# Kernel optimization log

Measured on AMD Instinct MI355X. Metric: run time of the kernel, lower is better.

## Reference

```python
import jax, jax.numpy as jnp
import numpy as np

B, L = 1, 384
D_EDGE, D_BIAS, N_HEAD, D_HEAD = 128, 64, 4, 48
INF = 1000000.0
SCALE = 1.0 / np.sqrt(D_HEAD)
EPS = 1e-5


def _layernorm(x, g, b):
    mu = jnp.mean(x, axis=-1, keepdims=True)
    var = jnp.mean(jnp.square(x - mu), axis=-1, keepdims=True)
    return (x - mu) * jax.lax.rsqrt(var + EPS) * g + b


def _rope(x, pos):
    # x: [B, n, L, h, d], pos: [B, L] integer positions along the attended (i/j) axis
    half = x.shape[-1] // 2
    inv_freq = 1.0 / (10000.0 ** (jnp.arange(half, dtype=jnp.float32) / half))
    ang = pos.astype(jnp.float32)[..., None] * inv_freq          # [B, L, half]
    cos = jnp.cos(ang)[:, None, :, None, :]                       # [B,1,L,1,half]
    sin = jnp.sin(ang)[:, None, :, None, :]
    x1, x2 = jnp.split(x, 2, axis=-1)
    return jnp.concatenate([x1 * cos - x2 * sin, x1 * sin + x2 * cos], axis=-1)


def setup_inputs() -> dict:
    key = jax.random.key(0)
    ks = jax.random.split(key, 10)
    s = 0.02
    return {
        "edge": jax.random.normal(ks[0], (B, L, L, D_EDGE), jnp.float32),
        "bias": jax.random.normal(ks[1], (B, L, L, D_BIAS), jnp.float32),
        "edge_pos": jnp.arange(B * L, dtype=jnp.int32).reshape(B, L),
        "edge_mask": jnp.ones((B, L, L), jnp.float32),
        "ln_e_g": jnp.ones((D_EDGE,), jnp.float32),
        "ln_e_b": jnp.zeros((D_EDGE,), jnp.float32),
        "ln_b_g": jnp.ones((D_BIAS,), jnp.float32),
        "ln_b_b": jnp.zeros((D_BIAS,), jnp.float32),
        "Wq": jax.random.normal(ks[2], (D_EDGE, N_HEAD * D_HEAD), jnp.float32) * s,
        "Wk": jax.random.normal(ks[3], (D_EDGE, N_HEAD * D_HEAD), jnp.float32) * s,
        "Wv": jax.random.normal(ks[4], (D_EDGE, N_HEAD * D_HEAD), jnp.float32) * s,
        "Wb": jax.random.normal(ks[5], (D_BIAS, N_HEAD), jnp.float32) * s,
        "Wg": jax.random.normal(ks[6], (D_EDGE, N_HEAD * D_HEAD), jnp.float32) * s,
        "bg": jnp.zeros((N_HEAD * D_HEAD,), jnp.float32),
        "Wo": jax.random.normal(ks[7], (N_HEAD * D_HEAD, D_EDGE), jnp.float32) * s,
    }


def reference(edge, bias, edge_pos, edge_mask, ln_e_g, ln_e_b, ln_b_g, ln_b_b,
              Wq, Wk, Wv, Wb, Wg, bg, Wo):
    # is_row=True: swap the two residue axes of the pair representation
    e = jnp.transpose(edge, (0, 2, 1, 3))
    bi = jnp.transpose(bias, (0, 2, 1, 3))
    e = _layernorm(e, ln_e_g, ln_e_b)
    bi = _layernorm(bi, ln_b_g, ln_b_b)

    def proj(x, W):
        return (x @ W).reshape(B, L, L, N_HEAD, D_HEAD)

    q = proj(e, Wq)                      # [B, n, i, h, d]
    k = proj(e, Wk)
    v = proj(e, Wv)
    q = _rope(q, edge_pos)
    k = _rope(k, edge_pos)
    b_h = bi @ Wb                        # [B, i, j, h]
    gate = jax.nn.sigmoid(proj(e, Wg) + bg.reshape(1, 1, 1, N_HEAD, D_HEAD))

    q = q * SCALE
    k = k / L
    attn = jnp.einsum('bnihk,bnjhk->bijh', q, k) + b_h
    attn = jax.nn.softmax(attn, axis=-2)                 # softmax over j (dim -2)
    attn = attn + (INF * (edge_mask - 1.0))[..., None]    # post-softmax additive mask

    out = jnp.einsum('bijh,bnjhd->bnihd', attn, v)        # [B, n, i, h, d]
    out = gate * out
    out = out.reshape(B, L, L, N_HEAD * D_HEAD) @ Wo      # [B, n, i, d_edge]
    return jnp.transpose(out, (0, 2, 1, 3))               # undo row permute
```

## Files before the change

### kernel.cpp

```cpp
#include <hip/hip_runtime.h>
#include <hip/hip_bf16.h>


#define LQ 384
#define DE 128
#define DBI 64
#define NH 4
#define DH 48
#define NPOS (LQ*LQ)
#define KQK (LQ*DH)
#define LDSS 72

typedef __attribute__((ext_vector_type(8))) short short8;
typedef __attribute__((ext_vector_type(4))) float f32x4;
typedef unsigned short u16;
typedef unsigned int u32;

__device__ __forceinline__ float b2f(u16 u) {
  union { u32 i; float f; } v; v.i = ((u32)u) << 16; return v.f;
}
__device__ __forceinline__ u16 f2b(float f) {
  __hip_bfloat16 h = __float2bfloat16(f);
  return __builtin_bit_cast(unsigned short, h);
}
__device__ __forceinline__ float wred_sum(float v) {
  #pragma unroll
  for (int o = 32; o; o >>= 1) v += __shfl_down(v, o);
  return __shfl(v, 0);
}

template<int NF>
__device__ __forceinline__ void gemm_loop(
    const u16* __restrict__ Ag, long lda,
    const u16* __restrict__ Bg, long ldb,
    int kTiles, u16* sA, u16* sB, f32x4 (&acc)[2][NF])
{
  const int t = threadIdx.x;
  const int w = t >> 6, lane = t & 63, quad = lane >> 4, l16 = lane & 15;
  for (int kt = 0; kt < kTiles; ++kt) {
    const u16* As = Ag + (long)kt * 64;
    #pragma unroll
    for (int r = 0; r < 4; ++r) {
      int id = t + r * 256;
      int row = id >> 3, c8 = (id & 7) * 8;
      *(uint4*)(sA + row * LDSS + c8) = *(const uint4*)(As + (long)row * lda + c8);
    }
    const u16* Bs = Bg + (long)kt * 64;
    #pragma unroll
    for (int r = 0; r < (NF * 128 + 255) / 256; ++r) {
      int id = t + r * 256;
      if (id < NF * 128) {
        int row = id >> 3, c8 = (id & 7) * 8;
        *(uint4*)(sB + row * LDSS + c8) = *(const uint4*)(Bs + (long)row * ldb + c8);
      }
    }
    __syncthreads();
    #pragma unroll
    for (int kk = 0; kk < 64; kk += 32) {
      short8 a0 = *(const short8*)(sA + (w * 32 + l16) * LDSS + kk + quad * 8);
      short8 a1 = *(const short8*)(sA + (w * 32 + 16 + l16) * LDSS + kk + quad * 8);
      #pragma unroll
      for (int f = 0; f < NF; ++f) {
        short8 bf = *(const short8*)(sB + (f * 16 + l16) * LDSS + kk + quad * 8);
        acc[0][f] = __builtin_amdgcn_mfma_f32_16x16x32_bf16(a0, bf, acc[0][f], 0, 0, 0);
        acc[1][f] = __builtin_amdgcn_mfma_f32_16x16x32_bf16(a1, bf, acc[1][f], 0, 0, 0);
      }
    }
    __syncthreads();
  }
}

__device__ __forceinline__ void gemm_loop_mul(
    const u16* __restrict__ A1, const u16* __restrict__ A2, long lda,
    const u16* __restrict__ Bg, long ldb,
    int kTiles, u16* sA, u16* sB, f32x4 (&acc)[2][4])
{
  const int t = threadIdx.x;
  const int w = t >> 6, lane = t & 63, quad = lane >> 4, l16 = lane & 15;
  for (int kt = 0; kt < kTiles; ++kt) {
    #pragma unroll
    for (int r = 0; r < 4; ++r) {
      int id = t + r * 256;
      int row = id >> 3, c8 = (id & 7) * 8;
      long off = (long)row * lda + kt * 64 + c8;
      union { u16 s[8]; uint4 v; } ua, ub, ur;
      ua.v = *(const uint4*)(A1 + off);
      ub.v = *(const uint4*)(A2 + off);
      #pragma unroll
      for (int q2 = 0; q2 < 8; ++q2) ur.s[q2] = f2b(b2f(ua.s[q2]) * b2f(ub.s[q2]));
      *(uint4*)(sA + row * LDSS + c8) = ur.v;
    }
    #pragma unroll
    for (int r = 0; r < 2; ++r) {
      int id = t + r * 256;
      int row = id >> 3, c8 = (id & 7) * 8;
      *(uint4*)(sB + row * LDSS + c8) = *(const uint4*)(Bg + (long)row * ldb + kt * 64 + c8);
    }
    __syncthreads();
    #pragma unroll
    for (int kk = 0; kk < 64; kk += 32) {
      short8 a0 = *(const short8*)(sA + (w * 32 + l16) * LDSS + kk + quad * 8);
      short8 a1 = *(const short8*)(sA + (w * 32 + 16 + l16) * LDSS + kk + quad * 8);
      #pragma unroll
      for (int f = 0; f < 4; ++f) {
        short8 bf = *(const short8*)(sB + (f * 16 + l16) * LDSS + kk + quad * 8);
        acc[0][f] = __builtin_amdgcn_mfma_f32_16x16x32_bf16(a0, bf, acc[0][f], 0, 0, 0);
        acc[1][f] = __builtin_amdgcn_mfma_f32_16x16x32_bf16(a1, bf, acc[1][f], 0, 0, 0);
      }
    }
    __syncthreads();
  }
}

__global__ __launch_bounds__(256) void k_prep_w(
    const float* __restrict__ Wq, const float* __restrict__ Wk,
    const float* __restrict__ Wv, const float* __restrict__ Wg,
    const float* __restrict__ Wo, u16* __restrict__ WT, u16* __restrict__ WoT)
{
  int idx = blockIdx.x * 256 + threadIdx.x;
  if (idx < 768 * 128) {
    int col = idx >> 7, c = idx & 127;
    int which = col / 192, wi = col % 192;
    const float* W = (which == 0) ? Wq : (which == 1) ? Wk : (which == 2) ? Wv : Wg;
    WT[(long)col * 128 + c] = f2b(W[(long)c * 192 + wi]);
  }
  if (idx < 128 * 192) {
    int c = idx / 192, col = idx % 192;
    WoT[(long)c * 192 + col] = f2b(Wo[(long)col * 128 + c]);
  }
}

__global__ __launch_bounds__(256) void k_ln_e(
    const float* __restrict__ edge, const float* __restrict__ g,
    const float* __restrict__ b, u16* __restrict__ e_ln)
{
  int w = threadIdx.x >> 6, lane = threadIdx.x & 63;
  long p = (long)blockIdx.x * 4 + w;
  int n = (int)(p / LQ), i2 = (int)(p % LQ);
  const float* src = edge + ((long)i2 * LQ + n) * DE;
  float2 x = *(const float2*)(src + lane * 2);
  float mu = wred_sum(x.x + x.y) * (1.f / 128.f);
  float ms = wred_sum(x.x * x.x + x.y * x.y) * (1.f / 128.f);
  float r = rsqrtf(ms - mu * mu + 1e-5f);
  int c = lane * 2;
  u16 y0 = f2b((x.x - mu) * r * g[c] + b[c]);
  u16 y1 = f2b((x.y - mu) * r * g[c + 1] + b[c + 1]);
  *(u32*)(e_ln + p * DE + c) = (u32)y0 | ((u32)y1 << 16);
}

__global__ __launch_bounds__(256) void k_bias(
    const float* __restrict__ bias, const float* __restrict__ g,
    const float* __restrict__ b, const float* __restrict__ Wb,
    float* __restrict__ logits)
{
  int w = threadIdx.x >> 6, lane = threadIdx.x & 63;
  long q = (long)blockIdx.x * 4 + w;
  int i = (int)(q / LQ), j = (int)(q % LQ);
  float x = bias[((long)j * LQ + i) * DBI + lane];
  float mu = wred_sum(x) * (1.f / 64.f);
  float ms = wred_sum(x * x) * (1.f / 64.f);
  float r = rsqrtf(ms - mu * mu + 1e-5f);
  float y = (x - mu) * r * g[lane] + b[lane];
  #pragma unroll
  for (int h = 0; h < 4; ++h) {
    float v = y * Wb[lane * 4 + h];
    #pragma unroll
    for (int o = 32; o; o >>= 1) v += __shfl_down(v, o);
    if (lane == 0) logits[((long)h * LQ + i) * LQ + j] = v;
  }
}

__global__ __launch_bounds__(256) void k_proj(
    const u16* __restrict__ e_ln, const u16* __restrict__ WT,
    const int* __restrict__ edge_pos, const float* __restrict__ bg,
    u16* __restrict__ q_buf, u16* __restrict__ k_buf,
    u16* __restrict__ vT, u16* __restrict__ gate)
{
  __shared__ u16 sA[128 * LDSS];
  __shared__ u16 sB[48 * LDSS];
  __shared__ float sC[128 * 49];
  int nt = blockIdx.x;
  long mt = blockIdx.y;
  int which = nt >> 2, h = nt & 3;
  f32x4 acc[2][3] = {};
  gemm_loop<3>(e_ln + mt * 128 * DE, DE, WT + (long)nt * 48 * DE, DE, 2, sA, sB, acc);
  const int t = threadIdx.x;
  const int w = t >> 6, lane = t & 63, quad = lane >> 4, l16 = lane & 15;
  #pragma unroll
  for (int rf = 0; rf < 2; ++rf)
    #pragma unroll
    for (int f = 0; f < 3; ++f)
      #pragma unroll
      for (int r = 0; r < 4; ++r)
        sC[(w * 32 + rf * 16 + quad * 4 + r) * 49 + f * 16 + l16] = acc[rf][f][r];
  __syncthreads();
  long pbase = mt * 128;
  int n = (int)(pbase / LQ);
  int i2base = (int)(pbase % LQ);
  if (which < 2) {
    float scl = (which == 0) ? 0.14433756729740643f : (1.0f / 384.0f);
    u16* dst = (which == 0) ? q_buf : k_buf;
    int row = t >> 1, half = t & 1;
    int i2 = i2base + row;
    float posf = (float)edge_pos[i2];
    long base = ((long)(h * LQ + i2) * LQ + n) * DH;
    #pragma unroll
    for (int kd = 0; kd < 24; kd += 2) {
      u16 y2[2];
      #pragma unroll
      for (int u = 0; u < 2; ++u) {
        int d = half * 24 + kd + u;
        int dd = (d < 24) ? d : d - 24;
        float ang = posf * exp2f((float)dd * (-13.287712379549449f / 24.f));
        float sn = sinf(ang), cs = cosf(ang);
        float x1 = sC[row * 49 + dd], x2 = sC[row * 49 + dd + 24];
        float y = (d < 24) ? (x1 * cs - x2 * sn) : (x1 * sn + x2 * cs);
        y2[u] = f2b(y * scl);
      }
      *(u32*)(dst + base + half * 24 + kd) = (u32)y2[0] | ((u32)y2[1] << 16);
    }
  } else if (which == 2) {
    for (int e = t; e < 6144; e += 256) {
      int d = e >> 7, row = e & 127;
      vT[((long)h * KQK + n * DH + d) * LQ + (i2base + row)] = f2b(sC[row * 49 + d]);
    }
  } else {
    for (int e = t; e < 6144; e += 256) {
      int row = e / 48, d = e - row * 48;
      float xx = sC[row * 49 + d] + bg[h * DH + d];
      gate[(pbase + row) * 192 + h * DH + d] = f2b(1.f / (1.f + expf(-xx)));
    }
  }
}

__global__ __launch_bounds__(256) void k_qk(
    const u16* __restrict__ q_buf, const u16* __restrict__ k_buf,
    float* __restrict__ logits)
{
  __shared__ u16 sA[128 * LDSS];
  __shared__ u16 sB[48 * LDSS];
  int nt = blockIdx.x & 7, s = blockIdx.x >> 3;
  int mt = blockIdx.y, h = blockIdx.z;
  f32x4 acc[2][3] = {};
  gemm_loop<3>(q_buf + ((long)h * LQ + mt * 128) * KQK + s * 2304, KQK,
               k_buf + ((long)h * LQ + nt * 48) * KQK + s * 2304, KQK,
               36, sA, sB, acc);
  const int t = threadIdx.x;
  const int w = t >> 6, lane = t & 63, quad = lane >> 4, l16 = lane & 15;
  #pragma unroll
  for (int rf = 0; rf < 2; ++rf)
    #pragma unroll
    for (int f = 0; f < 3; ++f)
      #pragma unroll
      for (int r = 0; r < 4; ++r) {
        int row = mt * 128 + w * 32 + rf * 16 + quad * 4 + r;
        int col = nt * 48 + f * 16 + l16;
        atomicAdd(logits + ((long)h * LQ + row) * LQ + col, acc[rf][f][r]);
      }
}

__global__ __launch_bounds__(256) void k_softmax(
    const float* __restrict__ logits, const float* __restrict__ mask,
    u16* __restrict__ attn)
{
  int w = threadIdx.x >> 6, lane = threadIdx.x & 63;
  long row = (long)blockIdx.x * 4 + w;
  int i = (int)(row % LQ);
  const float* src = logits + row * LQ;
  float v[6];
  float mx = -1e30f;
  #pragma unroll
  for (int j0 = 0; j0 < 6; ++j0) { v[j0] = src[lane + j0 * 64]; mx = fmaxf(mx, v[j0]); }
  #pragma unroll
  for (int o = 32; o; o >>= 1) mx = fmaxf(mx, __shfl_down(mx, o));
  mx = __shfl(mx, 0);
  float s = 0.f;
  #pragma unroll
  for (int j0 = 0; j0 < 6; ++j0) { v[j0] = expf(v[j0] - mx); s += v[j0]; }
  s = wred_sum(s);
  float inv = 1.f / s;
  #pragma unroll
  for (int j0 = 0; j0 < 6; ++j0) {
    int j = lane + j0 * 64;
    float p = v[j0] * inv + 1.0e6f * (mask[(long)i * LQ + j] - 1.f);
    attn[row * LQ + j] = f2b(p);
  }
}

__global__ __launch_bounds__(256) void k_av(
    const u16* __restrict__ attn, const u16* __restrict__ vT,
    u16* __restrict__ out_buf)
{
  __shared__ u16 sA[128 * LDSS];
  __shared__ u16 sB[48 * LDSS];
  int nt = blockIdx.x, mt = blockIdx.y, h = blockIdx.z;
  f32x4 acc[2][3] = {};
  gemm_loop<3>(attn + ((long)h * LQ + mt * 128) * LQ, LQ,
               vT + ((long)h * KQK + nt * DH) * LQ, LQ,
               6, sA, sB, acc);
  const int t = threadIdx.x;
  const int w = t >> 6, lane = t & 63, quad = lane >> 4, l16 = lane & 15;
  #pragma unroll
  for (int rf = 0; rf < 2; ++rf)
    #pragma unroll
    for (int f = 0; f < 3; ++f)
      #pragma unroll
      for (int r = 0; r < 4; ++r) {
        int i = mt * 128 + w * 32 + rf * 16 + quad * 4 + r;
        int d = f * 16 + l16;
        out_buf[((long)nt * LQ + i) * 192 + h * DH + d] = f2b(acc[rf][f][r]);
      }
}

__global__ __launch_bounds__(256) void k_out(
    const u16* __restrict__ out_buf, const u16* __restrict__ gate,
    const u16* __restrict__ WoT, float* __restrict__ outp)
{
  __shared__ u16 sA[128 * LDSS];
  __shared__ u16 sB[64 * LDSS];
  int nt = blockIdx.x;
  long mt = blockIdx.y;
  f32x4 acc[2][4] = {};
  gemm_loop_mul(out_buf + mt * 128 * 192, gate + mt * 128 * 192, 192,
                WoT + (long)nt * 64 * 192, 192, 3, sA, sB, acc);
  const int t = threadIdx.x;
  const int w = t >> 6, lane = t & 63, quad = lane >> 4, l16 = lane & 15;
  long pbase = mt * 128;
  int n = (int)(pbase / LQ), ibase = (int)(pbase % LQ);
  #pragma unroll
  for (int rf = 0; rf < 2; ++rf)
    #pragma unroll
    for (int f = 0; f < 4; ++f)
      #pragma unroll
      for (int r = 0; r < 4; ++r) {
        int row = w * 32 + rf * 16 + quad * 4 + r;
        int c = nt * 64 + f * 16 + l16;
        outp[((long)(ibase + row) * LQ + n) * DE + c] = acc[rf][f][r];
      }
}

extern "C" void kernel_launch(void* const* d_in, const int* in_sizes, int n_in,
                              void* d_out, int out_size, void* d_ws, size_t ws_size,
                              hipStream_t stream)
{
  const float* edge   = (const float*)d_in[0];
  const float* bias   = (const float*)d_in[1];
  const int*   epos   = (const int*)d_in[2];
  const float* mask   = (const float*)d_in[3];
  const float* ln_e_g = (const float*)d_in[4];
  const float* ln_e_b = (const float*)d_in[5];
  const float* ln_b_g = (const float*)d_in[6];
  const float* ln_b_b = (const float*)d_in[7];
  const float* Wq = (const float*)d_in[8];
  const float* Wk = (const float*)d_in[9];
  const float* Wv = (const float*)d_in[10];
  const float* Wb = (const float*)d_in[11];
  const float* Wg = (const float*)d_in[12];
  const float* bg = (const float*)d_in[13];
  const float* Wo = (const float*)d_in[14];
  float* outp = (float*)d_out;

  char* ws = (char*)d_ws;
  const size_t SZ = (size_t)NPOS * 192 * 2;
  u16* e_ln    = (u16*)ws;
  u16* out_buf = (u16*)ws;
  u16* q_buf   = (u16*)(ws + SZ);
  u16* k_buf   = (u16*)(ws + 2 * SZ);
  u16* vTb     = (u16*)(ws + 3 * SZ);
  u16* gateb   = (u16*)(ws + 4 * SZ);
  float* logits= (float*)(ws + 5 * SZ);
  u16* attn    = (u16*)(ws + 5 * SZ + 2359296);
  u16* WT      = (u16*)(ws + 5 * SZ + 2359296 + 1179648);
  u16* WoT     = (u16*)(ws + 5 * SZ + 2359296 + 1179648 + 196608);

  k_prep_w<<<dim3(384), dim3(256), 0, stream>>>(Wq, Wk, Wv, Wg, Wo, WT, WoT);
  k_ln_e<<<dim3(36864), dim3(256), 0, stream>>>(edge, ln_e_g, ln_e_b, e_ln);
  k_bias<<<dim3(36864), dim3(256), 0, stream>>>(bias, ln_b_g, ln_b_b, Wb, logits);
  k_proj<<<dim3(16, 1152), dim3(256), 0, stream>>>(e_ln, WT, epos, bg, q_buf, k_buf, vTb, gateb);
  k_qk<<<dim3(64, 3, 4), dim3(256), 0, stream>>>(q_buf, k_buf, logits);
  k_softmax<<<dim3(384), dim3(256), 0, stream>>>(logits, mask, attn);
  k_av<<<dim3(384, 3, 4), dim3(256), 0, stream>>>(attn, vTb, out_buf);
  k_out<<<dim3(2, 1152), dim3(256), 0, stream>>>(out_buf, gateb, WoT, outp);
}
```

Measured before the change: 684.8 us.

## Enlarge GEMM tiles, reuse A tile across projections, precompute RoPE tables

```diff
diff --git a/kernel.cpp b/kernel.cpp
--- a/kernel.cpp
+++ b/kernel.cpp
@@ -5,11 +5,9 @@
 #define LQ 384
 #define DE 128
 #define DBI 64
-#define NH 4
 #define DH 48
 #define NPOS (LQ*LQ)
 #define KQK (LQ*DH)
-#define LDSS 72
 
 typedef __attribute__((ext_vector_type(8))) short short8;
 typedef __attribute__((ext_vector_type(4))) float f32x4;
@@ -29,84 +27,39 @@
   return __shfl(v, 0);
 }
 
-template<int NF>
-__device__ __forceinline__ void gemm_loop(
-    const u16* __restrict__ Ag, long lda,
-    const u16* __restrict__ Bg, long ldb,
-    int kTiles, u16* sA, u16* sB, f32x4 (&acc)[2][NF])
+__device__ __forceinline__ void gemm_128x192(
+    const u16* __restrict__ A, long lda, const u16* __restrict__ B, long ldb,
+    int kTiles, u16* sA, u16* sB, f32x4 (&acc)[4][6])
 {
   const int t = threadIdx.x;
   const int w = t >> 6, lane = t & 63, quad = lane >> 4, l16 = lane & 15;
+  const int wr = w >> 1, wc = w & 1;
   for (int kt = 0; kt < kTiles; ++kt) {
-    const u16* As = Ag + (long)kt * 64;
     #pragma unroll
     for (int r = 0; r < 4; ++r) {
-      int id = t + r * 256;
-      int row = id >> 3, c8 = (id & 7) * 8;
-      *(uint4*)(sA + row * LDSS + c8) = *(const uint4*)(As + (long)row * lda + c8);
-    }
-    const u16* Bs = Bg + (long)kt * 64;
-    #pragma unroll
-    for (int r = 0; r < (NF * 128 + 255) / 256; ++r) {
-      int id = t + r * 256;
-      if (id < NF * 128) {
-        int row = id >> 3, c8 = (id & 7) * 8;
-        *(uint4*)(sB + row * LDSS + c8) = *(const uint4*)(Bs + (long)row * ldb + c8);
-      }
+      int id = t + r * 256, row = id >> 3, c8 = (id & 7) * 8;
+      *(uint4*)(sA + row * 72 + c8) = *(const uint4*)(A + (long)row * lda + kt * 64 + c8);
+    }
+    #pragma unroll
+    for (int r = 0; r < 6; ++r) {
+      int id = t + r * 256, row = id >> 3, c8 = (id & 7) * 8;
+      *(uint4*)(sB + row * 72 + c8) = *(const uint4*)(B + (long)row * ldb + kt * 64 + c8);
     }
     __syncthreads();
     #pragma unroll
     for (int kk = 0; kk < 64; kk += 32) {
-      short8 a0 = *(const short8*)(sA + (w * 32 + l16) * LDSS + kk + quad * 8);
-      short8 a1 = *(const short8*)(sA + (w * 32 + 16 + l16) * LDSS + kk + quad * 8);
-      #pragma unroll
-      for (int f = 0; f < NF; ++f) {
-        short8 bf = *(const short8*)(sB + (f * 16 + l16) * LDSS + kk + quad * 8);
-        acc[0][f] = __builtin_amdgcn_mfma_f32_16x16x32_bf16(a0, bf, acc[0][f], 0, 0, 0);
-        acc[1][f] = __builtin_amdgcn_mfma_f32_16x16x32_bf16(a1, bf, acc[1][f], 0, 0, 0);
-      }
-    }
-    __syncthreads();
-  }
-}
-
-__device__ __forceinline__ void gemm_loop_mul(
-    const u16* __restrict__ A1, const u16* __restrict__ A2, long lda,
-    const u16* __restrict__ Bg, long ldb,
-    int kTiles, u16* sA, u16* sB, f32x4 (&acc)[2][4])
-{
-  const int t = threadIdx.x;
-  const int w = t >> 6, lane = t & 63, quad = lane >> 4, l16 = lane & 15;
-  for (int kt = 0; kt < kTiles; ++kt) {
-    #pragma unroll
-    for (int r = 0; r < 4; ++r) {
-      int id = t + r * 256;
-      int row = id >> 3, c8 = (id & 7) * 8;
-      long off = (long)row * lda + kt * 64 + c8;
-      union { u16 s[8]; uint4 v; } ua, ub, ur;
-      ua.v = *(const uint4*)(A1 + off);
-      ub.v = *(const uint4*)(A2 + off);
-      #pragma unroll
-      for (int q2 = 0; q2 < 8; ++q2) ur.s[q2] = f2b(b2f(ua.s[q2]) * b2f(ub.s[q2]));
-      *(uint4*)(sA + row * LDSS + c8) = ur.v;
-    }
-    #pragma unroll
-    for (int r = 0; r < 2; ++r) {
-      int id = t + r * 256;
-      int row = id >> 3, c8 = (id & 7) * 8;
-      *(uint4*)(sB + row * LDSS + c8) = *(const uint4*)(Bg + (long)row * ldb + kt * 64 + c8);
-    }
-    __syncthreads();
-    #pragma unroll
-    for (int kk = 0; kk < 64; kk += 32) {
-      short8 a0 = *(const short8*)(sA + (w * 32 + l16) * LDSS + kk + quad * 8);
-      short8 a1 = *(const short8*)(sA + (w * 32 + 16 + l16) * LDSS + kk + quad * 8);
-      #pragma unroll
-      for (int f = 0; f < 4; ++f) {
-        short8 bf = *(const short8*)(sB + (f * 16 + l16) * LDSS + kk + quad * 8);
-        acc[0][f] = __builtin_amdgcn_mfma_f32_16x16x32_bf16(a0, bf, acc[0][f], 0, 0, 0);
-        acc[1][f] = __builtin_amdgcn_mfma_f32_16x16x32_bf16(a1, bf, acc[1][f], 0, 0, 0);
-      }
+      short8 a[4], bf[6];
+      #pragma unroll
+      for (int rr = 0; rr < 4; ++rr)
+        a[rr] = *(const short8*)(sA + (wr * 64 + rr * 16 + l16) * 72 + kk + quad * 8);
+      #pragma unroll
+      for (int f = 0; f < 6; ++f)
+        bf[f] = *(const short8*)(sB + (wc * 96 + f * 16 + l16) * 72 + kk + quad * 8);
+      #pragma unroll
+      for (int rr = 0; rr < 4; ++rr)
+        #pragma unroll
+        for (int f = 0; f < 6; ++f)
+          acc[rr][f] = __builtin_amdgcn_mfma_f32_16x16x32_bf16(a[rr], bf[f], acc[rr][f], 0, 0, 0);
     }
     __syncthreads();
   }
@@ -115,7 +68,9 @@
 __global__ __launch_bounds__(256) void k_prep_w(
     const float* __restrict__ Wq, const float* __restrict__ Wk,
     const float* __restrict__ Wv, const float* __restrict__ Wg,
-    const float* __restrict__ Wo, u16* __restrict__ WT, u16* __restrict__ WoT)
+    const float* __restrict__ Wo, const int* __restrict__ epos,
+    u16* __restrict__ WT, u16* __restrict__ WoT,
+    float* __restrict__ cosT, float* __restrict__ sinT)
 {
   int idx = blockIdx.x * 256 + threadIdx.x;
   if (idx < 768 * 128) {
@@ -127,6 +82,12 @@
   if (idx < 128 * 192) {
     int c = idx / 192, col = idx % 192;
     WoT[(long)c * 192 + col] = f2b(Wo[(long)col * 128 + c]);
+  }
+  if (idx < 384 * 24) {
+    int i2 = idx / 24, dd = idx % 24;
+    float ang = (float)epos[i2] * exp2f((float)dd * (-13.287712379549449f / 24.f));
+    cosT[idx] = cosf(ang);
+    sinT[idx] = sinf(ang);
   }
 }
 
@@ -172,64 +133,95 @@
 
 __global__ __launch_bounds__(256) void k_proj(
     const u16* __restrict__ e_ln, const u16* __restrict__ WT,
-    const int* __restrict__ edge_pos, const float* __restrict__ bg,
+    const float* __restrict__ cosT, const float* __restrict__ sinT,
+    const float* __restrict__ bg,
     u16* __restrict__ q_buf, u16* __restrict__ k_buf,
     u16* __restrict__ vT, u16* __restrict__ gate)
 {
-  __shared__ u16 sA[128 * LDSS];
-  __shared__ u16 sB[48 * LDSS];
-  __shared__ float sC[128 * 49];
-  int nt = blockIdx.x;
-  long mt = blockIdx.y;
-  int which = nt >> 2, h = nt & 3;
-  f32x4 acc[2][3] = {};
-  gemm_loop<3>(e_ln + mt * 128 * DE, DE, WT + (long)nt * 48 * DE, DE, 2, sA, sB, acc);
+  __shared__ __align__(16) u16 sA[128 * 136];
+  __shared__ __align__(16) char sU[128 * 49 * 4];
   const int t = threadIdx.x;
   const int w = t >> 6, lane = t & 63, quad = lane >> 4, l16 = lane & 15;
-  #pragma unroll
-  for (int rf = 0; rf < 2; ++rf)
-    #pragma unroll
-    for (int f = 0; f < 3; ++f)
-      #pragma unroll
-      for (int r = 0; r < 4; ++r)
-        sC[(w * 32 + rf * 16 + quad * 4 + r) * 49 + f * 16 + l16] = acc[rf][f][r];
+  long mt = blockIdx.x;
+  long pbase = mt * 128;
+  int n = (int)(pbase / LQ), i2base = (int)(pbase % LQ);
+
+  #pragma unroll
+  for (int r = 0; r < 8; ++r) {
+    int id = t + r * 256, row = id >> 4, c8 = (id & 15) * 8;
+    *(uint4*)(sA + row * 136 + c8) = *(const uint4*)(e_ln + (pbase + row) * DE + c8);
+  }
   __syncthreads();
-  long pbase = mt * 128;
-  int n = (int)(pbase / LQ);
-  int i2base = (int)(pbase % LQ);
-  if (which < 2) {
-    float scl = (which == 0) ? 0.14433756729740643f : (1.0f / 384.0f);
-    u16* dst = (which == 0) ? q_buf : k_buf;
-    int row = t >> 1, half = t & 1;
-    int i2 = i2base + row;
-    float posf = (float)edge_pos[i2];
-    long base = ((long)(h * LQ + i2) * LQ + n) * DH;
-    #pragma unroll
-    for (int kd = 0; kd < 24; kd += 2) {
-      u16 y2[2];
-      #pragma unroll
-      for (int u = 0; u < 2; ++u) {
-        int d = half * 24 + kd + u;
-        int dd = (d < 24) ? d : d - 24;
-        float ang = posf * exp2f((float)dd * (-13.287712379549449f / 24.f));
-        float sn = sinf(ang), cs = cosf(ang);
-        float x1 = sC[row * 49 + dd], x2 = sC[row * 49 + dd + 24];
-        float y = (d < 24) ? (x1 * cs - x2 * sn) : (x1 * sn + x2 * cs);
-        y2[u] = f2b(y * scl);
-      }
-      *(u32*)(dst + base + half * 24 + kd) = (u32)y2[0] | ((u32)y2[1] << 16);
-    }
-  } else if (which == 2) {
-    for (int e = t; e < 6144; e += 256) {
-      int d = e >> 7, row = e & 127;
-      vT[((long)h * KQK + n * DH + d) * LQ + (i2base + row)] = f2b(sC[row * 49 + d]);
-    }
-  } else {
-    for (int e = t; e < 6144; e += 256) {
-      int row = e / 48, d = e - row * 48;
-      float xx = sC[row * 49 + d] + bg[h * DH + d];
-      gate[(pbase + row) * 192 + h * DH + d] = f2b(1.f / (1.f + expf(-xx)));
-    }
+  short8 a[2][4];
+  #pragma unroll
+  for (int rr = 0; rr < 2; ++rr)
+    #pragma unroll
+    for (int kki = 0; kki < 4; ++kki)
+      a[rr][kki] = *(const short8*)(sA + (w * 32 + rr * 16 + l16) * 136 + kki * 32 + quad * 8);
+
+  for (int cc = 0; cc < 16; ++cc) {
+    int which = cc >> 2, h = cc & 3;
+    u16* sB = (u16*)sU;
+    #pragma unroll
+    for (int r = 0; r < 3; ++r) {
+      int id = t + r * 256, row = id >> 4, c8 = (id & 15) * 8;
+      *(uint4*)(sB + row * 136 + c8) = *(const uint4*)(WT + ((long)cc * 48 + row) * DE + c8);
+    }
+    __syncthreads();
+    f32x4 acc[2][3] = {};
+    #pragma unroll
+    for (int kki = 0; kki < 4; ++kki)
+      #pragma unroll
+      for (int f = 0; f < 3; ++f) {
+        short8 bf = *(const short8*)(sB + (f * 16 + l16) * 136 + kki * 32 + quad * 8);
+        acc[0][f] = __builtin_amdgcn_mfma_f32_16x16x32_bf16(a[0][kki], bf, acc[0][f], 0, 0, 0);
+        acc[1][f] = __builtin_amdgcn_mfma_f32_16x16x32_bf16(a[1][kki], bf, acc[1][f], 0, 0, 0);
+      }
+    __syncthreads();
+    float* sC = (float*)sU;
+    #pragma unroll
+    for (int rr = 0; rr < 2; ++rr)
+      #pragma unroll
+      for (int f = 0; f < 3; ++f)
+        #pragma unroll
+        for (int r = 0; r < 4; ++r)
+          sC[(w * 32 + rr * 16 + quad * 4 + r) * 49 + f * 16 + l16] = acc[rr][f][r];
+    __syncthreads();
+    if (which < 2) {
+      float scl = (which == 0) ? 0.14433756729740643f : (1.0f / 384.0f);
+      u16* dst = (which == 0) ? q_buf : k_buf;
+      int row = t >> 1, half = t & 1;
+      int i2 = i2base + row;
+      const float* ct = cosT + i2 * 24;
+      const float* st = sinT + i2 * 24;
+      long base = ((long)(h * LQ + i2) * LQ + n) * DH;
+      #pragma unroll
+      for (int kd = 0; kd < 24; kd += 2) {
+        u16 y2[2];
+        #pragma unroll
+        for (int u = 0; u < 2; ++u) {
+          int d = half * 24 + kd + u;
+          int dd = (d < 24) ? d : d - 24;
+          float cs = ct[dd], sn = st[dd];
+          float x1 = sC[row * 49 + dd], x2 = sC[row * 49 + dd + 24];
+          float y = (d < 24) ? (x1 * cs - x2 * sn) : (x1 * sn + x2 * cs);
+          y2[u] = f2b(y * scl);
+        }
+        *(u32*)(dst + base + half * 24 + kd) = (u32)y2[0] | ((u32)y2[1] << 16);
+      }
+    } else if (which == 2) {
+      for (int e = t; e < 6144; e += 256) {
+        int d = e >> 7, row = e & 127;
+        vT[((long)h * KQK + n * DH + d) * LQ + (i2base + row)] = f2b(sC[row * 49 + d]);
+      }
+    } else {
+      for (int e = t; e < 6144; e += 256) {
+        int row = e / 48, d = e - row * 48;
+        float xx = sC[row * 49 + d] + bg[h * DH + d];
+        gate[(pbase + row) * 192 + h * DH + d] = f2b(1.f / (1.f + expf(-xx)));
+      }
+    }
+    __syncthreads();
   }
 }
 
@@ -237,25 +229,26 @@
     const u16* __restrict__ q_buf, const u16* __restrict__ k_buf,
     float* __restrict__ logits)
 {
-  __shared__ u16 sA[128 * LDSS];
-  __shared__ u16 sB[48 * LDSS];
-  int nt = blockIdx.x & 7, s = blockIdx.x >> 3;
+  __shared__ __align__(16) u16 sA[128 * 72];
+  __shared__ __align__(16) u16 sB[192 * 72];
+  int nt = blockIdx.x & 1, s = blockIdx.x >> 1;
   int mt = blockIdx.y, h = blockIdx.z;
-  f32x4 acc[2][3] = {};
-  gemm_loop<3>(q_buf + ((long)h * LQ + mt * 128) * KQK + s * 2304, KQK,
-               k_buf + ((long)h * LQ + nt * 48) * KQK + s * 2304, KQK,
-               36, sA, sB, acc);
+  f32x4 acc[4][6] = {};
+  gemm_128x192(q_buf + ((long)h * LQ + mt * 128) * KQK + s * 576, KQK,
+               k_buf + ((long)h * LQ + nt * 192) * KQK + s * 576, KQK,
+               9, sA, sB, acc);
   const int t = threadIdx.x;
   const int w = t >> 6, lane = t & 63, quad = lane >> 4, l16 = lane & 15;
-  #pragma unroll
-  for (int rf = 0; rf < 2; ++rf)
-    #pragma unroll
-    for (int f = 0; f < 3; ++f)
+  const int wr = w >> 1, wc = w & 1;
+  #pragma unroll
+  for (int rr = 0; rr < 4; ++rr)
+    #pragma unroll
+    for (int f = 0; f < 6; ++f)
       #pragma unroll
       for (int r = 0; r < 4; ++r) {
-        int row = mt * 128 + w * 32 + rf * 16 + quad * 4 + r;
-        int col = nt * 48 + f * 16 + l16;
-        atomicAdd(logits + ((long)h * LQ + row) * LQ + col, acc[rf][f][r]);
+        int row = mt * 128 + wr * 64 + rr * 16 + quad * 4 + r;
+        int col = nt * 192 + wc * 96 + f * 16 + l16;
+        atomicAdd(logits + ((long)h * LQ + row) * LQ + col, acc[rr][f][r]);
       }
 }
 
@@ -291,24 +284,26 @@
     const u16* __restrict__ attn, const u16* __restrict__ vT,
     u16* __restrict__ out_buf)
 {
-  __shared__ u16 sA[128 * LDSS];
-  __shared__ u16 sB[48 * LDSS];
+  __shared__ __align__(16) u16 sA[128 * 72];
+  __shared__ __align__(16) u16 sB[192 * 72];
   int nt = blockIdx.x, mt = blockIdx.y, h = blockIdx.z;
-  f32x4 acc[2][3] = {};
-  gemm_loop<3>(attn + ((long)h * LQ + mt * 128) * LQ, LQ,
-               vT + ((long)h * KQK + nt * DH) * LQ, LQ,
+  f32x4 acc[4][6] = {};
+  gemm_128x192(attn + ((long)h * LQ + mt * 128) * LQ, LQ,
+               vT + ((long)h * KQK + nt * 192) * LQ, LQ,
                6, sA, sB, acc);
   const int t = threadIdx.x;
   const int w = t >> 6, lane = t & 63, quad = lane >> 4, l16 = lane & 15;
-  #pragma unroll
-  for (int rf = 0; rf < 2; ++rf)
-    #pragma unroll
-    for (int f = 0; f < 3; ++f)
+  const int wr = w >> 1, wc = w & 1;
+  #pragma unroll
+  for (int rr = 0; rr < 4; ++rr)
+    #pragma unroll
+    for (int f = 0; f < 6; ++f)
       #pragma unroll
       for (int r = 0; r < 4; ++r) {
-        int i = mt * 128 + w * 32 + rf * 16 + quad * 4 + r;
-        int d = f * 16 + l16;
-        out_buf[((long)nt * LQ + i) * 192 + h * DH + d] = f2b(acc[rf][f][r]);
+        int i = mt * 128 + wr * 64 + rr * 16 + quad * 4 + r;
+        int C = nt * 192 + wc * 96 + f * 16 + l16;
+        int nn = C / 48, d = C - nn * 48;
+        out_buf[((long)nn * LQ + i) * 192 + h * DH + d] = f2b(acc[rr][f][r]);
       }
 }
 
@@ -316,26 +311,61 @@
     const u16* __restrict__ out_buf, const u16* __restrict__ gate,
     const u16* __restrict__ WoT, float* __restrict__ outp)
 {
-  __shared__ u16 sA[128 * LDSS];
-  __shared__ u16 sB[64 * LDSS];
-  int nt = blockIdx.x;
-  long mt = blockIdx.y;
-  f32x4 acc[2][4] = {};
-  gemm_loop_mul(out_buf + mt * 128 * 192, gate + mt * 128 * 192, 192,
-                WoT + (long)nt * 64 * 192, 192, 3, sA, sB, acc);
+  __shared__ __align__(16) u16 sA[128 * 72];
+  __shared__ __align__(16) u16 sB[128 * 72];
+  long mt = blockIdx.x;
   const int t = threadIdx.x;
   const int w = t >> 6, lane = t & 63, quad = lane >> 4, l16 = lane & 15;
+  const int wr = w >> 1, wc = w & 1;
+  f32x4 acc[4][4] = {};
+  const u16* A1 = out_buf + mt * 128 * 192;
+  const u16* A2 = gate + mt * 128 * 192;
+  for (int kt = 0; kt < 3; ++kt) {
+    #pragma unroll
+    for (int r = 0; r < 4; ++r) {
+      int id = t + r * 256, row = id >> 3, c8 = (id & 7) * 8;
+      long off = (long)row * 192 + kt * 64 + c8;
+      union { u16 s[8]; uint4 v; } ua, ub, ur;
+      ua.v = *(const uint4*)(A1 + off);
+      ub.v = *(const uint4*)(A2 + off);
+      #pragma unroll
+      for (int q2 = 0; q2 < 8; ++q2) ur.s[q2] = f2b(b2f(ua.s[q2]) * b2f(ub.s[q2]));
+      *(uint4*)(sA + row * 72 + c8) = ur.v;
+    }
+    #pragma unroll
+    for (int r = 0; r < 4; ++r) {
+      int id = t + r * 256, row = id >> 3, c8 = (id & 7) * 8;
+      *(uint4*)(sB + row * 72 + c8) = *(const uint4*)(WoT + (long)row * 192 + kt * 64 + c8);
+    }
+    __syncthreads();
+    #pragma unroll
+    for (int kk = 0; kk < 64; kk += 32) {
+      short8 a[4], bf[4];
+      #pragma unroll
+      for (int rr = 0; rr < 4; ++rr)
+        a[rr] = *(const short8*)(sA + (wr * 64 + rr * 16 + l16) * 72 + kk + quad * 8);
+      #pragma unroll
+      for (int f = 0; f < 4; ++f)
+        bf[f] = *(const short8*)(sB + (wc * 64 + f * 16 + l16) * 72 + kk + quad * 8);
+      #pragma unroll
+      for (int rr = 0; rr < 4; ++rr)
+        #pragma unroll
+        for (int f = 0; f < 4; ++f)
+          acc[rr][f] = __builtin_amdgcn_mfma_f32_16x16x32_bf16(a[rr], bf[f], acc[rr][f], 0, 0, 0);
+    }
+    __syncthreads();
+  }
   long pbase = mt * 128;
   int n = (int)(pbase / LQ), ibase = (int)(pbase % LQ);
   #pragma unroll
-  for (int rf = 0; rf < 2; ++rf)
+  for (int rr = 0; rr < 4; ++rr)
     #pragma unroll
     for (int f = 0; f < 4; ++f)
       #pragma unroll
       for (int r = 0; r < 4; ++r) {
-        int row = w * 32 + rf * 16 + quad * 4 + r;
-        int c = nt * 64 + f * 16 + l16;
-        outp[((long)(ibase + row) * LQ + n) * DE + c] = acc[rf][f][r];
+        int row = wr * 64 + rr * 16 + quad * 4 + r;
+        int c = wc * 64 + f * 16 + l16;
+        outp[((long)(ibase + row) * LQ + n) * DE + c] = acc[rr][f][r];
       }
 }
 
@@ -372,13 +402,15 @@
   u16* attn    = (u16*)(ws + 5 * SZ + 2359296);
   u16* WT      = (u16*)(ws + 5 * SZ + 2359296 + 1179648);
   u16* WoT     = (u16*)(ws + 5 * SZ + 2359296 + 1179648 + 196608);
-
-  k_prep_w<<<dim3(384), dim3(256), 0, stream>>>(Wq, Wk, Wv, Wg, Wo, WT, WoT);
+  float* cosT  = (float*)(ws + 5 * SZ + 2359296 + 1179648 + 196608 + 49152);
+  float* sinT  = cosT + 384 * 24;
+
+  k_prep_w<<<dim3(384), dim3(256), 0, stream>>>(Wq, Wk, Wv, Wg, Wo, epos, WT, WoT, cosT, sinT);
   k_ln_e<<<dim3(36864), dim3(256), 0, stream>>>(edge, ln_e_g, ln_e_b, e_ln);
   k_bias<<<dim3(36864), dim3(256), 0, stream>>>(bias, ln_b_g, ln_b_b, Wb, logits);
-  k_proj<<<dim3(16, 1152), dim3(256), 0, stream>>>(e_ln, WT, epos, bg, q_buf, k_buf, vTb, gateb);
+  k_proj<<<dim3(1152), dim3(256), 0, stream>>>(e_ln, WT, cosT, sinT, bg, q_buf, k_buf, vTb, gateb);
   k_qk<<<dim3(64, 3, 4), dim3(256), 0, stream>>>(q_buf, k_buf, logits);
   k_softmax<<<dim3(384), dim3(256), 0, stream>>>(logits, mask, attn);
-  k_av<<<dim3(384, 3, 4), dim3(256), 0, stream>>>(attn, vTb, out_buf);
-  k_out<<<dim3(2, 1152), dim3(256), 0, stream>>>(out_buf, gateb, WoT, outp);
-}
+  k_av<<<dim3(96, 3, 4), dim3(256), 0, stream>>>(attn, vTb, out_buf);
+  k_out<<<dim3(1152), dim3(256), 0, stream>>>(out_buf, gateb, WoT, outp);
+}
```

Measured after the change: 579.1 us. -15.4%, faster.
